# Optimization experiments

Hardware: AMD Instinct MI355X
Metric: run time of the kernel (lower is better)

Reference implementation:

```python
import jax, jax.numpy as jnp
import numpy as np

N = 10000
E = 160000
IN_CH, HID, OUT = 14, 128, 4
HEADS = 8
NEG_SLOPE = 0.2


def setup_inputs() -> dict:
    key = jax.random.key(0)
    ks = jax.random.split(key, 16)
    glorot = lambda k, shape: jax.random.normal(k, shape, jnp.float32) * np.sqrt(2.0 / (shape[0] + shape[-1]))
    inp = {
        'x': jax.random.normal(ks[0], (N, IN_CH), jnp.float32),
        'edge_index': jax.random.randint(ks[1], (2, E), 0, N, jnp.int64),
        # layer 1: 14 -> 8 heads x 128, concat
        'W1': glorot(ks[2], (IN_CH, HEADS * HID)),
        'a_src1': glorot(ks[3], (HEADS, HID)),
        'a_dst1': glorot(ks[4], (HEADS, HID)),
        'b1': jnp.zeros((HEADS * HID,), jnp.float32),
        # layer 2: 1024 -> 8 heads x 128, concat
        'W2': glorot(ks[5], (HEADS * HID, HEADS * HID)),
        'a_src2': glorot(ks[6], (HEADS, HID)),
        'a_dst2': glorot(ks[7], (HEADS, HID)),
        'b2': jnp.zeros((HEADS * HID,), jnp.float32),
        # layer 3: 1024 -> 1 head x 4, mean (concat=False)
        'W3': glorot(ks[8], (HEADS * HID, OUT)),
        'a_src3': glorot(ks[9], (1, OUT)),
        'a_dst3': glorot(ks[10], (1, OUT)),
        'b3': jnp.zeros((OUT,), jnp.float32),
    }
    return inp


def gat_conv(x, src, dst, W, a_src, a_dst, b, heads, out_ch, concat):
    n = x.shape[0]
    h = (x @ W).reshape(n, heads, out_ch)                      # [N,H,C]
    al_s = jnp.sum(h * a_src, axis=-1)                         # [N,H]
    al_d = jnp.sum(h * a_dst, axis=-1)                         # [N,H]
    e = al_s[src] + al_d[dst]                                  # [E,H]
    e = jnp.where(e > 0, e, NEG_SLOPE * e)                     # LeakyReLU(0.2)
    # segment softmax over incoming edges of each dst node
    m = jax.ops.segment_max(e, dst, num_segments=n)
    ex = jnp.exp(e - m[dst])
    z = jax.ops.segment_sum(ex, dst, num_segments=n)
    alpha = ex / (z[dst] + 1e-16)                              # [E,H]
    out = jax.ops.segment_sum(h[src] * alpha[:, :, None], dst, num_segments=n)  # [N,H,C]
    out = out.reshape(n, heads * out_ch) if concat else out.mean(axis=1)
    return out + b


def reference(x, edge_index, W1, a_src1, a_dst1, b1, W2, a_src2, a_dst2, b2, W3, a_src3, a_dst3, b3):
    n = x.shape[0]
    # add self-loops (PyG GATConv default)
    loop = jnp.arange(n, dtype=edge_index.dtype)
    src = jnp.concatenate([edge_index[0], loop])
    dst = jnp.concatenate([edge_index[1], loop])
    # dropout layers are identity in eval mode
    h = gat_conv(x, src, dst, W1, a_src1, a_dst1, b1, HEADS, HID, True)
    h = jax.nn.relu(h)
    h = gat_conv(h, src, dst, W2, a_src2, a_dst2, b2, HEADS, HID, True)
    h = jax.nn.relu(h)
    h = gat_conv(h, src, dst, W3, a_src3, a_dst3, b3, 1, OUT, False)
    h = jax.nn.relu(h)
    return h
```

## Files before the change

kernel.cpp:

```cpp
#include <hip/hip_runtime.h>

typedef unsigned short ushort_t;
typedef unsigned int uint32;

#define N_NODES 10000
#define N_EDGES 160000
#define ET (N_NODES + N_EDGES)
#define MPAD 10112
#define HT 1024
#define HEADS 8
#define NEG 0.2f
#define AGG_CH 64

#define O_FLAG     0
#define O_SRC      256
#define O_DST      (O_SRC + 680192)
#define O_COUNTS   (O_DST + 680192)
#define O_OFFS     (O_COUNTS + 40192)
#define O_CURS     (O_OFFS + 40192)
#define O_SSORT    (O_CURS + 40192)
#define O_ALS      (O_SSORT + 680192)
#define O_ALD      (O_ALS + 320000)
#define O_AL3S     (O_ALD + 320000)
#define O_AL3D     (O_AL3S + 40192)
#define O_H3       (O_AL3D + 40192)
#define O_XF       (O_H3 + 160000)
#define O_W1F      (O_XF + 560128)
#define O_AS1F     (O_W1F + 57344)
#define O_W3F      (O_AS1F + 24576)
#define O_S3F      (O_W3F + 16384)
#define O_W2T      (O_S3F + 768)
#define O_BUFA     (O_W2T + 2097152)
#define O_BUFB     (O_BUFA + 20709376)

__device__ __forceinline__ float bf2f(ushort_t u){ return __uint_as_float(((uint32)u) << 16); }
__device__ __forceinline__ ushort_t f2bf(float f){
    uint32 x = __float_as_uint(f);
    return (ushort_t)((x + 0x7fffu + ((x >> 16) & 1u)) >> 16);
}
__device__ __forceinline__ void unpack2(uint32 u, float& lo, float& hi){
    lo = __uint_as_float(u << 16);
    hi = __uint_as_float(u & 0xffff0000u);
}

typedef __bf16 bf16x8 __attribute__((ext_vector_type(8)));
typedef float  f32x4  __attribute__((ext_vector_type(4)));

typedef const __attribute__((address_space(1))) uint32* gas1_u32;
typedef       __attribute__((address_space(3))) uint32* las3_u32;

__device__ __forceinline__ void gload_lds16(const void* g, void* l){
    __builtin_amdgcn_global_load_lds((gas1_u32)g, (las3_u32)l, 16, 0, 0);
}

__global__ void k_probe(const int* __restrict__ ei, const uint32* __restrict__ w1raw,
                        int* __restrict__ flags){
    if (threadIdx.x == 0){
        int nz = 0;
        for (int i = 0; i < 128; i++) nz |= ei[2*i + 1];
        flags[0] = (nz == 0) ? 1 : 0;
    }
    if (threadIdx.x == 1){
        int cnt = 0;
        for (int i = 0; i < 256; i++){
            uint32 e = (w1raw[i] >> 7) & 0xffu;
            cnt += (e >= 64u && e <= 160u) ? 1 : 0;
        }
        flags[1] = (cnt > 200) ? 0 : 1;
    }
}

struct CvtArgs {
    const void* src[12];
    float*      dst[12];
    int         n[12];
};

__global__ __launch_bounds__(256) void k_cvt(CvtArgs a, const int* __restrict__ flags){
    int aid = blockIdx.y;
    int n = a.n[aid];
    int base = blockIdx.x * 1024 + threadIdx.x * 4;
    if (base >= n) return;
    int f32 = flags[1];
    const void* s = a.src[aid];
    float* d = a.dst[aid];
    #pragma unroll
    for (int j = 0; j < 4; j++){
        int i = base + j;
        if (i < n){
            d[i] = f32 ? ((const float*)s)[i] : bf2f(((const ushort_t*)s)[i]);
        }
    }
}

__global__ __launch_bounds__(256) void k_extract_hist(const void* __restrict__ ei, const int* __restrict__ flags,
                                                      int* __restrict__ src, int* __restrict__ dst,
                                                      int* __restrict__ counts){
    int i = blockIdx.x * 256 + threadIdx.x;
    int is64 = flags[0];
    int s = -1, d = -1;
    if (i < N_EDGES){
        if (is64){
            const long long* p = (const long long*)ei;
            s = (int)p[i]; d = (int)p[N_EDGES + i];
        } else {
            const int* p = (const int*)ei;
            s = p[i]; d = p[N_EDGES + i];
        }
    } else if (i < ET){
        s = i - N_EDGES; d = s;
    }
    if (d >= 0){
        src[i] = s; dst[i] = d;
        atomicAdd(&counts[d], 1);
    }
}

__global__ __launch_bounds__(1024) void k_scan(const int* __restrict__ counts, int* __restrict__ offs,
                                               int* __restrict__ cursors, int n){
    __shared__ int wsum[16];
    __shared__ int running_s;
    int tid = threadIdx.x;
    int lane = tid & 63, wid = tid >> 6;
    if (tid == 0) running_s = 0;
    __syncthreads();
    for (int base = 0; base < n; base += 1024){
        int i = base + tid;
        int v = (i < n) ? counts[i] : 0;
        int x = v;
        #pragma unroll
        for (int d = 1; d < 64; d <<= 1){
            int t = __shfl_up(x, d, 64);
            if (lane >= d) x += t;
        }
        if (lane == 63) wsum[wid] = x;
        __syncthreads();
        if (wid == 0 && lane < 16){
            int w = wsum[lane];
            #pragma unroll
            for (int d = 1; d < 16; d <<= 1){
                int t = __shfl_up(w, d, 64);
                if (lane >= d) w += t;
            }
            wsum[lane] = w;
        }
        __syncthreads();
        int wprefix = (wid == 0) ? 0 : wsum[wid - 1];
        int run = running_s;
        int excl = run + wprefix + (x - v);
        if (i < n){ offs[i] = excl; cursors[i] = excl; }
        __syncthreads();
        if (tid == 0) running_s = run + wsum[15];
        __syncthreads();
    }
    if (tid == 0) offs[n] = running_s;
}

__global__ __launch_bounds__(256) void k_scatter(const int* __restrict__ src, const int* __restrict__ dst,
                                                 int* __restrict__ cursors, int* __restrict__ ssort){
    int i = blockIdx.x * 256 + threadIdx.x;
    if (i < ET){
        int pos = atomicAdd(&cursors[dst[i]], 1);
        ssort[pos] = src[i];
    }
}

__global__ __launch_bounds__(256) void k_gemm1f(const float* __restrict__ x, const float* __restrict__ W1,
                                                const float* __restrict__ a_src, const float* __restrict__ a_dst,
                                                ushort_t* __restrict__ h1,
                                                float* __restrict__ alS, float* __restrict__ alD){
    __shared__ float w1s[14 * HT];
    int tid = threadIdx.x;
    for (int i = tid * 4; i < 14 * HT; i += 1024)
        *(float4*)(w1s + i) = *(const float4*)(W1 + i);
    int c0 = tid * 4;
    float4 sv = *(const float4*)(a_src + c0);
    float4 dv = *(const float4*)(a_dst + c0);
    int head = tid >> 5, l32 = tid & 31;
    __syncthreads();
    for (int n = blockIdx.x; n < N_NODES; n += gridDim.x){
        float a0=0.f, a1=0.f, a2=0.f, a3=0.f;
        #pragma unroll
        for (int k = 0; k < 14; k++){
            float xv = x[n*14 + k];
            float4 w = *(const float4*)(w1s + k*HT + c0);
            a0 += xv*w.x; a1 += xv*w.y; a2 += xv*w.z; a3 += xv*w.w;
        }
        uint2 o;
        o.x = (uint32)f2bf(a0) | ((uint32)f2bf(a1) << 16);
        o.y = (uint32)f2bf(a2) | ((uint32)f2bf(a3) << 16);
        *(uint2*)(h1 + (size_t)n*HT + c0) = o;
        float h0,h1v,h2,h3v;
        unpack2(o.x, h0, h1v); unpack2(o.y, h2, h3v);
        float s = h0*sv.x + h1v*sv.y + h2*sv.z + h3v*sv.w;
        float d = h0*dv.x + h1v*dv.y + h2*dv.z + h3v*dv.w;
        #pragma unroll
        for (int of = 16; of; of >>= 1){ s += __shfl_xor(s, of, 32); d += __shfl_xor(d, of, 32); }
        if (l32 == 0){ alS[n*HEADS + head] = s; alD[n*HEADS + head] = d; }
    }
}

__global__ __launch_bounds__(256) void k_alpha2(const ushort_t* __restrict__ H, const float* __restrict__ a_src,
                                                const float* __restrict__ a_dst,
                                                float* __restrict__ alS, float* __restrict__ alD){
    int tid = threadIdx.x;
    int c0 = tid * 4;
    float4 sv = *(const float4*)(a_src + c0);
    float4 dv = *(const float4*)(a_dst + c0);
    int head = tid >> 5, l32 = tid & 31;
    int n0 = blockIdx.x * 16;
    for (int i = 0; i < 16; i++){
        int n = n0 + i;
        uint2 hv = *(const uint2*)(H + (size_t)n*HT + c0);
        float h0,h1,h2,h3;
        unpack2(hv.x, h0, h1); unpack2(hv.y, h2, h3);
        float s = h0*sv.x + h1*sv.y + h2*sv.z + h3*sv.w;
        float d = h0*dv.x + h1*dv.y + h2*dv.z + h3*dv.w;
        #pragma unroll
        for (int of = 16; of; of >>= 1){ s += __shfl_xor(s, of, 32); d += __shfl_xor(d, of, 32); }
        if (l32 == 0){ alS[n*HEADS + head] = s; alD[n*HEADS + head] = d; }
    }
}

__global__ __launch_bounds__(256) void k_gat_agg(const ushort_t* __restrict__ H, const float* __restrict__ alS,
                                                 const float* __restrict__ alD, const int* __restrict__ offs,
                                                 const int* __restrict__ srcs, const float* __restrict__ bias,
                                                 ushort_t* __restrict__ out){
    int n = blockIdx.x;
    int tid = threadIdx.x;
    int beg = offs[n], end = offs[n+1];
    __shared__ float sm[HEADS], sz[HEADS];
    __shared__ int   sE[AGG_CH];
    __shared__ float wE[AGG_CH][HEADS];
    __shared__ float red[HEADS][128];

    {
        int head32 = tid >> 5, l32 = tid & 31;
        float ad = alD[n*HEADS + head32];
        float m = -1e30f;
        for (int e = beg + l32; e < end; e += 32){
            float v = alS[srcs[e]*HEADS + head32] + ad;
            v = v > 0.f ? v : NEG*v;
            m = fmaxf(m, v);
        }
        #pragma unroll
        for (int o = 16; o; o >>= 1) m = fmaxf(m, __shfl_xor(m, o, 32));
        float z = 0.f;
        for (int e = beg + l32; e < end; e += 32){
            float v = alS[srcs[e]*HEADS + head32] + ad;
            v = v > 0.f ? v : NEG*v;
            z += __expf(v - m);
        }
        #pragma unroll
        for (int o = 16; o; o >>= 1) z += __shfl_xor(z, o, 32);
        if (l32 == 0){ sm[head32] = m; sz[head32] = z; }
    }
    __syncthreads();

    int slot = tid >> 7;
    int lt   = tid & 127;
    int ch0  = lt * 8;
    int head = lt >> 4;
    float acc[8];
    #pragma unroll
    for (int j = 0; j < 8; j++) acc[j] = 0.f;

    for (int cb = beg; cb < end; cb += AGG_CH){
        int cn = min(AGG_CH, end - cb);
        if (tid < cn) sE[tid] = srcs[cb + tid];
        __syncthreads();
        #pragma unroll
        for (int r = 0; r < 2; r++){
            int idx = tid + r*256;
            int e = idx >> 3, hd = idx & 7;
            if (e < cn){
                int s = sE[e];
                float v = alS[s*HEADS + hd] + alD[n*HEADS + hd];
                v = v > 0.f ? v : NEG*v;
                wE[e][hd] = __expf(v - sm[hd]) / (sz[hd] + 1e-16f);
            }
        }
        __syncthreads();
        for (int e = slot; e < cn; e += 2){
            int s = sE[e];
            float w = wE[e][head];
            uint4 hv = *(const uint4*)(H + (size_t)s*HT + ch0);
            float f0,f1,f2,f3,f4,f5,f6,f7;
            unpack2(hv.x, f0, f1); unpack2(hv.y, f2, f3);
            unpack2(hv.z, f4, f5); unpack2(hv.w, f6, f7);
            acc[0]+=w*f0; acc[1]+=w*f1; acc[2]+=w*f2; acc[3]+=w*f3;
            acc[4]+=w*f4; acc[5]+=w*f5; acc[6]+=w*f6; acc[7]+=w*f7;
        }
        __syncthreads();
    }
    if (slot == 1){
        #pragma unroll
        for (int j = 0; j < 8; j++) red[j & 7][lt] = acc[j] + 0.f*red[0][0];
    }
    __syncthreads();
    if (slot == 0){
        #pragma unroll
        for (int j = 0; j < 8; j++) acc[j] += red[j][lt];
        float4 bv0 = *(const float4*)(bias + ch0);
        float4 bv1 = *(const float4*)(bias + ch0 + 4);
        float r0 = fmaxf(acc[0]+bv0.x, 0.f), r1 = fmaxf(acc[1]+bv0.y, 0.f);
        float r2 = fmaxf(acc[2]+bv0.z, 0.f), r3 = fmaxf(acc[3]+bv0.w, 0.f);
        float r4 = fmaxf(acc[4]+bv1.x, 0.f), r5 = fmaxf(acc[5]+bv1.y, 0.f);
        float r6 = fmaxf(acc[6]+bv1.z, 0.f), r7 = fmaxf(acc[7]+bv1.w, 0.f);
        uint4 o;
        o.x = (uint32)f2bf(r0) | ((uint32)f2bf(r1) << 16);
        o.y = (uint32)f2bf(r2) | ((uint32)f2bf(r3) << 16);
        o.z = (uint32)f2bf(r4) | ((uint32)f2bf(r5) << 16);
        o.w = (uint32)f2bf(r6) | ((uint32)f2bf(r7) << 16);
        *(uint4*)(out + (size_t)n*HT + ch0) = o;
    }
}

__global__ __launch_bounds__(256) void k_transpose(const void* __restrict__ in, const int* __restrict__ flags,
                                                   ushort_t* __restrict__ out){
    __shared__ ushort_t tile[32][33];
    int f32 = flags[1];
    int bx = blockIdx.x, by = blockIdx.y;
    int cx = threadIdx.x & 31;
    int ry = (threadIdx.x >> 5) * 4;
    #pragma unroll
    for (int r = 0; r < 4; r++){
        size_t idx = (size_t)(by*32 + ry + r)*1024 + bx*32 + cx;
        tile[ry + r][cx] = f32 ? f2bf(((const float*)in)[idx]) : ((const ushort_t*)in)[idx];
    }
    __syncthreads();
    #pragma unroll
    for (int r = 0; r < 4; r++)
        out[(size_t)(bx*32 + ry + r)*1024 + by*32 + cx] = tile[cx][ry + r];
}

__global__ __launch_bounds__(256) void k_gemm2(const ushort_t* __restrict__ A, const ushort_t* __restrict__ BT,
                                               ushort_t* __restrict__ C){
    __shared__ ushort_t lA[128*32];
    __shared__ ushort_t lB[128*32];
    int tid = threadIdx.x;
    int bm = blockIdx.x, bn = blockIdx.y;
    int lane = tid & 63;
    int wave = tid >> 6;
    int wm = (wave & 1) * 64, wn = (wave >> 1) * 64;
    int lm = lane & 15, kg = lane >> 4;
    f32x4 acc[4][4];
    #pragma unroll
    for (int i = 0; i < 4; i++)
        #pragma unroll
        for (int j = 0; j < 4; j++) acc[i][j] = (f32x4)0.0f;

    const int K = 1024;
    int rowA0 = bm * 128, rowB0 = bn * 128;
    for (int k0 = 0; k0 < K; k0 += 32){
        #pragma unroll
        for (int it = 0; it < 2; ++it){
            int s = tid + it*256;
            int r = s >> 2, ks = s & 3;
            gload_lds16(A  + (size_t)(rowA0 + r)*K + k0 + ks*8, lA + s*8);
            gload_lds16(BT + (size_t)(rowB0 + r)*K + k0 + ks*8, lB + s*8);
        }
        __syncthreads();
        bf16x8 af[4], bfr[4];
        #pragma unroll
        for (int mt = 0; mt < 4; mt++) af[mt]  = *(const bf16x8*)(lA + (wm + mt*16 + lm)*32 + kg*8);
        #pragma unroll
        for (int nt = 0; nt < 4; nt++) bfr[nt] = *(const bf16x8*)(lB + (wn + nt*16 + lm)*32 + kg*8);
        #pragma unroll
        for (int mt = 0; mt < 4; mt++)
            #pragma unroll
            for (int nt = 0; nt < 4; nt++)
                acc[mt][nt] = __builtin_amdgcn_mfma_f32_16x16x32_bf16(af[mt], bfr[nt], acc[mt][nt], 0, 0, 0);
        __syncthreads();
    }
    #pragma unroll
    for (int mt = 0; mt < 4; mt++){
        int row_base = bm*128 + wm + mt*16 + kg*4;
        #pragma unroll
        for (int nt = 0; nt < 4; nt++){
            int col = bn*128 + wn + nt*16 + lm;
            #pragma unroll
            for (int r = 0; r < 4; r++){
                int row = row_base + r;
                if (row < N_NODES) C[(size_t)row*HT + col] = f2bf(acc[mt][nt][r]);
            }
        }
    }
}

__global__ __launch_bounds__(256) void k_gemm3(const ushort_t* __restrict__ A, const float* __restrict__ W3,
                                               const float* __restrict__ s3,
                                               float* __restrict__ h3, float* __restrict__ al3s, float* __restrict__ al3d){
    int tid = threadIdx.x;
    int lane = tid & 63, wave = tid >> 6;
    int n = blockIdx.x * 4 + wave;
    if (n >= N_NODES) return;
    float4 w3r[16];
    #pragma unroll
    for (int j = 0; j < 16; j++) w3r[j] = ((const float4*)W3)[lane*16 + j];
    const uint4* ap = (const uint4*)(A + (size_t)n*HT + lane*16);
    uint4 u0 = ap[0], u1 = ap[1];
    uint32 uu[8] = {u0.x,u0.y,u0.z,u0.w,u1.x,u1.y,u1.z,u1.w};
    float acc0=0.f, acc1=0.f, acc2=0.f, acc3=0.f;
    #pragma unroll
    for (int p = 0; p < 8; p++){
        float lo, hi;
        unpack2(uu[p], lo, hi);
        float4 wl = w3r[p*2], wh = w3r[p*2+1];
        acc0 += lo*wl.x + hi*wh.x;
        acc1 += lo*wl.y + hi*wh.y;
        acc2 += lo*wl.z + hi*wh.z;
        acc3 += lo*wl.w + hi*wh.w;
    }
    #pragma unroll
    for (int o = 32; o; o >>= 1){
        acc0 += __shfl_xor(acc0, o, 64); acc1 += __shfl_xor(acc1, o, 64);
        acc2 += __shfl_xor(acc2, o, 64); acc3 += __shfl_xor(acc3, o, 64);
    }
    if (lane == 0){
        *(float4*)(h3 + n*4) = make_float4(acc0, acc1, acc2, acc3);
        al3s[n] = acc0*s3[0] + acc1*s3[1] + acc2*s3[2] + acc3*s3[3];
        al3d[n] = acc0*s3[16] + acc1*s3[17] + acc2*s3[18] + acc3*s3[19];
    }
}

__global__ __launch_bounds__(256) void k_gat_agg3(const float* __restrict__ h3, const float* __restrict__ al3s,
                                                  const float* __restrict__ al3d, const int* __restrict__ offs,
                                                  const int* __restrict__ srcs, const float* __restrict__ b3,
                                                  const int* __restrict__ flags, void* __restrict__ out){
    int tid = threadIdx.x;
    int l = tid & 63, wave = tid >> 6;
    int n = blockIdx.x * 4 + wave;
    if (n >= N_NODES) return;
    int beg = offs[n], end = offs[n+1];
    float ad = al3d[n];
    float m = -1e30f;
    for (int e = beg + l; e < end; e += 64){
        float v = al3s[srcs[e]] + ad; v = v > 0.f ? v : NEG*v;
        m = fmaxf(m, v);
    }
    #pragma unroll
    for (int o = 32; o; o >>= 1) m = fmaxf(m, __shfl_xor(m, o, 64));
    float z = 0.f;
    for (int e = beg + l; e < end; e += 64){
        float v = al3s[srcs[e]] + ad; v = v > 0.f ? v : NEG*v;
        z += __expf(v - m);
    }
    #pragma unroll
    for (int o = 32; o; o >>= 1) z += __shfl_xor(z, o, 64);
    float inv = 1.f / (z + 1e-16f);
    float a0=0.f, a1=0.f, a2=0.f, a3=0.f;
    for (int e = beg + l; e < end; e += 64){
        int s = srcs[e];
        float v = al3s[s] + ad; v = v > 0.f ? v : NEG*v;
        float w = __expf(v - m) * inv;
        float4 hv = *(const float4*)(h3 + s*4);
        a0 += w*hv.x; a1 += w*hv.y; a2 += w*hv.z; a3 += w*hv.w;
    }
    #pragma unroll
    for (int o = 32; o; o >>= 1){
        a0 += __shfl_xor(a0, o, 64); a1 += __shfl_xor(a1, o, 64);
        a2 += __shfl_xor(a2, o, 64); a3 += __shfl_xor(a3, o, 64);
    }
    if (l == 0){
        float r0 = fmaxf(a0 + b3[0], 0.f);
        float r1 = fmaxf(a1 + b3[1], 0.f);
        float r2 = fmaxf(a2 + b3[2], 0.f);
        float r3 = fmaxf(a3 + b3[3], 0.f);
        if (flags[1]){
            float* o4 = (float*)out;
            o4[n*4+0]=r0; o4[n*4+1]=r1; o4[n*4+2]=r2; o4[n*4+3]=r3;
        } else {
            ushort_t* o2 = (ushort_t*)out;
            o2[n*4+0]=f2bf(r0); o2[n*4+1]=f2bf(r1); o2[n*4+2]=f2bf(r2); o2[n*4+3]=f2bf(r3);
        }
    }
}

extern "C" void kernel_launch(void* const* d_in, const int* in_sizes, int n_in,
                              void* d_out, int out_size, void* d_ws, size_t ws_size,
                              hipStream_t stream){
    const void* x   = d_in[0];
    const void* ei  = d_in[1];
    const void* W1  = d_in[2];
    const void* as1 = d_in[3];
    const void* ad1 = d_in[4];
    const void* b1  = d_in[5];
    const void* W2  = d_in[6];
    const void* as2 = d_in[7];
    const void* ad2 = d_in[8];
    const void* b2  = d_in[9];
    const void* W3  = d_in[10];
    const void* as3 = d_in[11];
    const void* ad3 = d_in[12];
    const void* b3  = d_in[13];

    char* ws = (char*)d_ws;
    int* flags     = (int*)(ws + O_FLAG);
    int* srcA      = (int*)(ws + O_SRC);
    int* dstA      = (int*)(ws + O_DST);
    int* counts    = (int*)(ws + O_COUNTS);
    int* offs      = (int*)(ws + O_OFFS);
    int* cursors   = (int*)(ws + O_CURS);
    int* ssort     = (int*)(ws + O_SSORT);
    float* alS     = (float*)(ws + O_ALS);
    float* alD     = (float*)(ws + O_ALD);
    float* al3s    = (float*)(ws + O_AL3S);
    float* al3d    = (float*)(ws + O_AL3D);
    float* h3      = (float*)(ws + O_H3);
    float* xF      = (float*)(ws + O_XF);
    float* W1F     = (float*)(ws + O_W1F);
    float* wvecF   = (float*)(ws + O_AS1F);
    float* W3F     = (float*)(ws + O_W3F);
    float* s3F     = (float*)(ws + O_S3F);
    ushort_t* W2T  = (ushort_t*)(ws + O_W2T);
    ushort_t* bufA = (ushort_t*)(ws + O_BUFA);
    ushort_t* bufB = (ushort_t*)(ws + O_BUFB);

    const int EB = (ET + 255) / 256;

    k_probe<<<1, 64, 0, stream>>>((const int*)ei, (const uint32*)W1, flags);

    CvtArgs ca;
    ca.src[0]=x;   ca.dst[0]=xF;            ca.n[0]=140000;
    ca.src[1]=W1;  ca.dst[1]=W1F;           ca.n[1]=14336;
    ca.src[2]=as1; ca.dst[2]=wvecF+0*1024;  ca.n[2]=1024;
    ca.src[3]=ad1; ca.dst[3]=wvecF+1*1024;  ca.n[3]=1024;
    ca.src[4]=b1;  ca.dst[4]=wvecF+2*1024;  ca.n[4]=1024;
    ca.src[5]=as2; ca.dst[5]=wvecF+3*1024;  ca.n[5]=1024;
    ca.src[6]=ad2; ca.dst[6]=wvecF+4*1024;  ca.n[6]=1024;
    ca.src[7]=b2;  ca.dst[7]=wvecF+5*1024;  ca.n[7]=1024;
    ca.src[8]=W3;  ca.dst[8]=W3F;           ca.n[8]=4096;
    ca.src[9]=as3; ca.dst[9]=s3F+0;         ca.n[9]=4;
    ca.src[10]=ad3; ca.dst[10]=s3F+16;      ca.n[10]=4;
    ca.src[11]=b3;  ca.dst[11]=s3F+32;      ca.n[11]=4;
    k_cvt<<<dim3(137, 12), 256, 0, stream>>>(ca, flags);

    hipMemsetAsync(counts, 0, N_NODES*sizeof(int), stream);
    k_extract_hist<<<EB, 256, 0, stream>>>(ei, flags, srcA, dstA, counts);
    k_scan<<<1, 1024, 0, stream>>>(counts, offs, cursors, N_NODES);
    k_scatter<<<EB, 256, 0, stream>>>(srcA, dstA, cursors, ssort);

    k_gemm1f<<<512, 256, 0, stream>>>(xF, W1F, wvecF+0*1024, wvecF+1*1024, bufA, alS, alD);
    k_gat_agg<<<N_NODES, 256, 0, stream>>>(bufA, alS, alD, offs, ssort, wvecF+2*1024, bufB);

    k_transpose<<<dim3(32, 32), 256, 0, stream>>>(W2, flags, W2T);
    k_gemm2<<<dim3(79, 8), 256, 0, stream>>>(bufB, W2T, bufA);
    k_alpha2<<<625, 256, 0, stream>>>(bufA, wvecF+3*1024, wvecF+4*1024, alS, alD);
    k_gat_agg<<<N_NODES, 256, 0, stream>>>(bufA, alS, alD, offs, ssort, wvecF+5*1024, bufB);

    k_gemm3<<<2500, 256, 0, stream>>>(bufB, W3F, s3F, h3, al3s, al3d);
    k_gat_agg3<<<2500, 256, 0, stream>>>(h3, al3s, al3d, offs, ssort, s3F+32, flags, d_out);
}
```

Measured before the change: 334.5 us.

## Fuse setup kernels, fold alpha into GEMM2, rewrite GAT aggregation with online softmax

Merges the probe, conversion, counts memset and W2 transpose into one setup kernel, so fewer launches are serialized. The per-node attention logits for layer 2 are now computed in the GEMM2 epilogue from fp32 accumulators, which removes the separate alpha pass over H. The aggregation kernel is rewritten to use two waves per node with shuffle-broadcast sources and an online max/sum softmax, avoiding LDS staging and block barriers. Risks include redundant probe_f32 work in every setup block and an extra reduction and barrier in the GEMM2 epilogue.

```diff
diff --git a/kernel.cpp b/kernel.cpp
--- a/kernel.cpp
+++ b/kernel.cpp
@@ -10,7 +10,6 @@
 #define HT 1024
 #define HEADS 8
 #define NEG 0.2f
-#define AGG_CH 64
 
 #define O_FLAG     0
 #define O_SRC      256
@@ -53,21 +52,18 @@
     __builtin_amdgcn_global_load_lds((gas1_u32)g, (las3_u32)l, 16, 0, 0);
 }
 
-__global__ void k_probe(const int* __restrict__ ei, const uint32* __restrict__ w1raw,
-                        int* __restrict__ flags){
-    if (threadIdx.x == 0){
-        int nz = 0;
-        for (int i = 0; i < 128; i++) nz |= ei[2*i + 1];
-        flags[0] = (nz == 0) ? 1 : 0;
-    }
-    if (threadIdx.x == 1){
-        int cnt = 0;
-        for (int i = 0; i < 256; i++){
-            uint32 e = (w1raw[i] >> 7) & 0xffu;
-            cnt += (e >= 64u && e <= 160u) ? 1 : 0;
-        }
-        flags[1] = (cnt > 200) ? 0 : 1;
-    }
+__device__ __forceinline__ int probe_f32(const uint32* __restrict__ w){
+    int cnt = 0;
+    for (int i = 0; i < 256; i++){
+        uint32 e = (w[i] >> 7) & 0xffu;
+        cnt += (e >= 64u && e <= 160u) ? 1 : 0;
+    }
+    return (cnt > 200) ? 0 : 1;
+}
+__device__ __forceinline__ int probe_edge64(const int* __restrict__ ei){
+    int nz = 0;
+    for (int i = 0; i < 128; i++) nz |= ei[2*i + 1];
+    return (nz == 0) ? 1 : 0;
 }
 
 struct CvtArgs {
@@ -76,20 +72,55 @@
     int         n[12];
 };
 
-__global__ __launch_bounds__(256) void k_cvt(CvtArgs a, const int* __restrict__ flags){
-    int aid = blockIdx.y;
-    int n = a.n[aid];
-    int base = blockIdx.x * 1024 + threadIdx.x * 4;
-    if (base >= n) return;
-    int f32 = flags[1];
-    const void* s = a.src[aid];
-    float* d = a.dst[aid];
-    #pragma unroll
-    for (int j = 0; j < 4; j++){
-        int i = base + j;
-        if (i < n){
-            d[i] = f32 ? ((const float*)s)[i] : bf2f(((const ushort_t*)s)[i]);
-        }
+__global__ __launch_bounds__(256) void k_setup(CvtArgs a, const void* __restrict__ W2,
+                                               const uint32* __restrict__ w1raw,
+                                               const int* __restrict__ eiraw,
+                                               int* __restrict__ counts,
+                                               ushort_t* __restrict__ W2T,
+                                               int* __restrict__ flags){
+    __shared__ ushort_t tile[32][33];
+    int slice = blockIdx.y;
+    int tid = threadIdx.x;
+    if (slice < 12){
+        int n = a.n[slice];
+        int base = blockIdx.x * 1024 + tid * 4;
+        if (base >= n) return;
+        int f32 = probe_f32(w1raw);
+        const void* s = a.src[slice];
+        float* d = a.dst[slice];
+        #pragma unroll
+        for (int j = 0; j < 4; j++){
+            int i = base + j;
+            if (i < n) d[i] = f32 ? ((const float*)s)[i] : bf2f(((const ushort_t*)s)[i]);
+        }
+    } else if (slice == 12){
+        if (blockIdx.x == 10){
+            if (tid == 0) flags[0] = probe_edge64(eiraw);
+            if (tid == 1) flags[1] = probe_f32(w1raw);
+            return;
+        }
+        if (blockIdx.x < 10){
+            int i0 = blockIdx.x * 1024 + tid * 4;
+            if (i0 + 3 < N_NODES){
+                *(int4*)(counts + i0) = make_int4(0,0,0,0);
+            } else {
+                for (int j = 0; j < 4; j++) if (i0 + j < N_NODES) counts[i0 + j] = 0;
+            }
+        }
+    } else {
+        int f32 = probe_f32(w1raw);
+        int bx = blockIdx.x & 31, by = blockIdx.x >> 5;
+        int cx = tid & 31;
+        int ry = (tid >> 5) * 4;
+        #pragma unroll
+        for (int r = 0; r < 4; r++){
+            size_t idx = (size_t)(by*32 + ry + r)*1024 + bx*32 + cx;
+            tile[ry + r][cx] = f32 ? f2bf(((const float*)W2)[idx]) : ((const ushort_t*)W2)[idx];
+        }
+        __syncthreads();
+        #pragma unroll
+        for (int r = 0; r < 4; r++)
+            W2T[(size_t)(bx*32 + ry + r)*1024 + by*32 + cx] = tile[cx][ry + r];
     }
 }
 
@@ -200,144 +231,100 @@
     }
 }
 
-__global__ __launch_bounds__(256) void k_alpha2(const ushort_t* __restrict__ H, const float* __restrict__ a_src,
-                                                const float* __restrict__ a_dst,
-                                                float* __restrict__ alS, float* __restrict__ alD){
-    int tid = threadIdx.x;
-    int c0 = tid * 4;
-    float4 sv = *(const float4*)(a_src + c0);
-    float4 dv = *(const float4*)(a_dst + c0);
-    int head = tid >> 5, l32 = tid & 31;
-    int n0 = blockIdx.x * 16;
-    for (int i = 0; i < 16; i++){
-        int n = n0 + i;
-        uint2 hv = *(const uint2*)(H + (size_t)n*HT + c0);
-        float h0,h1,h2,h3;
-        unpack2(hv.x, h0, h1); unpack2(hv.y, h2, h3);
-        float s = h0*sv.x + h1*sv.y + h2*sv.z + h3*sv.w;
-        float d = h0*dv.x + h1*dv.y + h2*dv.z + h3*dv.w;
-        #pragma unroll
-        for (int of = 16; of; of >>= 1){ s += __shfl_xor(s, of, 32); d += __shfl_xor(d, of, 32); }
-        if (l32 == 0){ alS[n*HEADS + head] = s; alD[n*HEADS + head] = d; }
-    }
-}
-
 __global__ __launch_bounds__(256) void k_gat_agg(const ushort_t* __restrict__ H, const float* __restrict__ alS,
                                                  const float* __restrict__ alD, const int* __restrict__ offs,
                                                  const int* __restrict__ srcs, const float* __restrict__ bias,
                                                  ushort_t* __restrict__ out){
-    int n = blockIdx.x;
-    int tid = threadIdx.x;
+    int tid = threadIdx.x;
+    int wv = tid >> 6, lane = tid & 63;
+    int n = blockIdx.x * 2 + (wv >> 1);
+    int half = wv & 1;
     int beg = offs[n], end = offs[n+1];
-    __shared__ float sm[HEADS], sz[HEADS];
-    __shared__ int   sE[AGG_CH];
-    __shared__ float wE[AGG_CH][HEADS];
-    __shared__ float red[HEADS][128];
-
-    {
-        int head32 = tid >> 5, l32 = tid & 31;
-        float ad = alD[n*HEADS + head32];
-        float m = -1e30f;
-        for (int e = beg + l32; e < end; e += 32){
-            float v = alS[srcs[e]*HEADS + head32] + ad;
+    int head = half*4 + (lane >> 4);
+    int slot = lane & 15;
+    float ad = alD[n*HEADS + head];
+
+    float m = -1e30f, z = 0.f;
+    for (int c = beg; c < end; c += 64){
+        int cn = min(64, end - c);
+        int sreg = (lane < cn) ? srcs[c + lane] : 0;
+        for (int p = slot; p < cn; p += 16){
+            int s = __shfl(sreg, p, 64);
+            float v = alS[s*HEADS + head] + ad;
             v = v > 0.f ? v : NEG*v;
-            m = fmaxf(m, v);
-        }
-        #pragma unroll
-        for (int o = 16; o; o >>= 1) m = fmaxf(m, __shfl_xor(m, o, 32));
-        float z = 0.f;
-        for (int e = beg + l32; e < end; e += 32){
-            float v = alS[srcs[e]*HEADS + head32] + ad;
-            v = v > 0.f ? v : NEG*v;
-            z += __expf(v - m);
-        }
-        #pragma unroll
-        for (int o = 16; o; o >>= 1) z += __shfl_xor(z, o, 32);
-        if (l32 == 0){ sm[head32] = m; sz[head32] = z; }
-    }
-    __syncthreads();
-
-    int slot = tid >> 7;
-    int lt   = tid & 127;
-    int ch0  = lt * 8;
-    int head = lt >> 4;
-    float acc[8];
-    #pragma unroll
-    for (int j = 0; j < 8; j++) acc[j] = 0.f;
-
-    for (int cb = beg; cb < end; cb += AGG_CH){
-        int cn = min(AGG_CH, end - cb);
-        if (tid < cn) sE[tid] = srcs[cb + tid];
-        __syncthreads();
-        #pragma unroll
-        for (int r = 0; r < 2; r++){
-            int idx = tid + r*256;
-            int e = idx >> 3, hd = idx & 7;
-            if (e < cn){
-                int s = sE[e];
-                float v = alS[s*HEADS + hd] + alD[n*HEADS + hd];
-                v = v > 0.f ? v : NEG*v;
-                wE[e][hd] = __expf(v - sm[hd]) / (sz[hd] + 1e-16f);
-            }
-        }
-        __syncthreads();
-        for (int e = slot; e < cn; e += 2){
-            int s = sE[e];
-            float w = wE[e][head];
-            uint4 hv = *(const uint4*)(H + (size_t)s*HT + ch0);
+            if (v > m){ z = z*__expf(m - v) + 1.f; m = v; }
+            else z += __expf(v - m);
+        }
+    }
+    #pragma unroll
+    for (int o = 1; o < 16; o <<= 1){
+        float m2 = __shfl_xor(m, o, 64);
+        float z2 = __shfl_xor(z, o, 64);
+        float nm = fmaxf(m, m2);
+        z = z*__expf(m - nm) + z2*__expf(m2 - nm);
+        m = nm;
+    }
+    float inv = 1.f / (z + 1e-16f);
+
+    int ch0 = half*512 + lane*8;
+    const ushort_t* Hc = H + ch0;
+    float c0=0.f,c1=0.f,c2=0.f,c3=0.f,c4=0.f,c5=0.f,c6=0.f,c7=0.f;
+    for (int c = beg; c < end; c += 64){
+        int cn = min(64, end - c);
+        int sreg = (lane < cn) ? srcs[c + lane] : 0;
+        int j = 0;
+        for (; j + 2 <= cn; j += 2){
+            int s0 = __shfl(sreg, j, 64);
+            int s1 = __shfl(sreg, j+1, 64);
+            uint4 u0 = *(const uint4*)(Hc + (size_t)s0*HT);
+            uint4 u1 = *(const uint4*)(Hc + (size_t)s1*HT);
+            float v0 = alS[s0*HEADS + head] + ad;
+            float v1 = alS[s1*HEADS + head] + ad;
+            v0 = v0 > 0.f ? v0 : NEG*v0;
+            v1 = v1 > 0.f ? v1 : NEG*v1;
+            float w0 = __expf(v0 - m) * inv;
+            float w1 = __expf(v1 - m) * inv;
             float f0,f1,f2,f3,f4,f5,f6,f7;
-            unpack2(hv.x, f0, f1); unpack2(hv.y, f2, f3);
-            unpack2(hv.z, f4, f5); unpack2(hv.w, f6, f7);
-            acc[0]+=w*f0; acc[1]+=w*f1; acc[2]+=w*f2; acc[3]+=w*f3;
-            acc[4]+=w*f4; acc[5]+=w*f5; acc[6]+=w*f6; acc[7]+=w*f7;
-        }
-        __syncthreads();
-    }
-    if (slot == 1){
-        #pragma unroll
-        for (int j = 0; j < 8; j++) red[j & 7][lt] = acc[j] + 0.f*red[0][0];
-    }
-    __syncthreads();
-    if (slot == 0){
-        #pragma unroll
-        for (int j = 0; j < 8; j++) acc[j] += red[j][lt];
-        float4 bv0 = *(const float4*)(bias + ch0);
-        float4 bv1 = *(const float4*)(bias + ch0 + 4);
-        float r0 = fmaxf(acc[0]+bv0.x, 0.f), r1 = fmaxf(acc[1]+bv0.y, 0.f);
-        float r2 = fmaxf(acc[2]+bv0.z, 0.f), r3 = fmaxf(acc[3]+bv0.w, 0.f);
-        float r4 = fmaxf(acc[4]+bv1.x, 0.f), r5 = fmaxf(acc[5]+bv1.y, 0.f);
-        float r6 = fmaxf(acc[6]+bv1.z, 0.f), r7 = fmaxf(acc[7]+bv1.w, 0.f);
-        uint4 o;
-        o.x = (uint32)f2bf(r0) | ((uint32)f2bf(r1) << 16);
-        o.y = (uint32)f2bf(r2) | ((uint32)f2bf(r3) << 16);
-        o.z = (uint32)f2bf(r4) | ((uint32)f2bf(r5) << 16);
-        o.w = (uint32)f2bf(r6) | ((uint32)f2bf(r7) << 16);
-        *(uint4*)(out + (size_t)n*HT + ch0) = o;
-    }
-}
-
-__global__ __launch_bounds__(256) void k_transpose(const void* __restrict__ in, const int* __restrict__ flags,
-                                                   ushort_t* __restrict__ out){
-    __shared__ ushort_t tile[32][33];
-    int f32 = flags[1];
-    int bx = blockIdx.x, by = blockIdx.y;
-    int cx = threadIdx.x & 31;
-    int ry = (threadIdx.x >> 5) * 4;
-    #pragma unroll
-    for (int r = 0; r < 4; r++){
-        size_t idx = (size_t)(by*32 + ry + r)*1024 + bx*32 + cx;
-        tile[ry + r][cx] = f32 ? f2bf(((const float*)in)[idx]) : ((const ushort_t*)in)[idx];
-    }
-    __syncthreads();
-    #pragma unroll
-    for (int r = 0; r < 4; r++)
-        out[(size_t)(bx*32 + ry + r)*1024 + by*32 + cx] = tile[cx][ry + r];
+            unpack2(u0.x,f0,f1); unpack2(u0.y,f2,f3); unpack2(u0.z,f4,f5); unpack2(u0.w,f6,f7);
+            c0+=w0*f0; c1+=w0*f1; c2+=w0*f2; c3+=w0*f3;
+            c4+=w0*f4; c5+=w0*f5; c6+=w0*f6; c7+=w0*f7;
+            unpack2(u1.x,f0,f1); unpack2(u1.y,f2,f3); unpack2(u1.z,f4,f5); unpack2(u1.w,f6,f7);
+            c0+=w1*f0; c1+=w1*f1; c2+=w1*f2; c3+=w1*f3;
+            c4+=w1*f4; c5+=w1*f5; c6+=w1*f6; c7+=w1*f7;
+        }
+        if (j < cn){
+            int s0 = __shfl(sreg, j, 64);
+            uint4 u0 = *(const uint4*)(Hc + (size_t)s0*HT);
+            float v0 = alS[s0*HEADS + head] + ad;
+            v0 = v0 > 0.f ? v0 : NEG*v0;
+            float w0 = __expf(v0 - m) * inv;
+            float f0,f1,f2,f3,f4,f5,f6,f7;
+            unpack2(u0.x,f0,f1); unpack2(u0.y,f2,f3); unpack2(u0.z,f4,f5); unpack2(u0.w,f6,f7);
+            c0+=w0*f0; c1+=w0*f1; c2+=w0*f2; c3+=w0*f3;
+            c4+=w0*f4; c5+=w0*f5; c6+=w0*f6; c7+=w0*f7;
+        }
+    }
+    float4 b0 = *(const float4*)(bias + ch0);
+    float4 b1 = *(const float4*)(bias + ch0 + 4);
+    c0 = fmaxf(c0+b0.x, 0.f); c1 = fmaxf(c1+b0.y, 0.f);
+    c2 = fmaxf(c2+b0.z, 0.f); c3 = fmaxf(c3+b0.w, 0.f);
+    c4 = fmaxf(c4+b1.x, 0.f); c5 = fmaxf(c5+b1.y, 0.f);
+    c6 = fmaxf(c6+b1.z, 0.f); c7 = fmaxf(c7+b1.w, 0.f);
+    uint4 o;
+    o.x = (uint32)f2bf(c0) | ((uint32)f2bf(c1) << 16);
+    o.y = (uint32)f2bf(c2) | ((uint32)f2bf(c3) << 16);
+    o.z = (uint32)f2bf(c4) | ((uint32)f2bf(c5) << 16);
+    o.w = (uint32)f2bf(c6) | ((uint32)f2bf(c7) << 16);
+    *(uint4*)(out + (size_t)n*HT + ch0) = o;
 }
 
 __global__ __launch_bounds__(256) void k_gemm2(const ushort_t* __restrict__ A, const ushort_t* __restrict__ BT,
-                                               ushort_t* __restrict__ C){
+                                               ushort_t* __restrict__ C,
+                                               const float* __restrict__ aS, const float* __restrict__ aD,
+                                               float* __restrict__ alS, float* __restrict__ alD){
     __shared__ ushort_t lA[128*32];
     __shared__ ushort_t lB[128*32];
+    __shared__ float reds[2][64][2];
     int tid = threadIdx.x;
     int bm = blockIdx.x, bn = blockIdx.y;
     int lane = tid & 63;
@@ -383,6 +370,46 @@
             for (int r = 0; r < 4; r++){
                 int row = row_base + r;
                 if (row < N_NODES) C[(size_t)row*HT + col] = f2bf(acc[mt][nt][r]);
+            }
+        }
+    }
+    float as_l[4], ad_l[4];
+    #pragma unroll
+    for (int nt = 0; nt < 4; nt++){
+        as_l[nt] = aS[bn*128 + wn + nt*16 + lm];
+        ad_l[nt] = aD[bn*128 + wn + nt*16 + lm];
+    }
+    float psA[4][4], pdA[4][4];
+    #pragma unroll
+    for (int mt = 0; mt < 4; mt++){
+        #pragma unroll
+        for (int r = 0; r < 4; r++){
+            float ps = acc[mt][0][r]*as_l[0] + acc[mt][1][r]*as_l[1]
+                     + acc[mt][2][r]*as_l[2] + acc[mt][3][r]*as_l[3];
+            float pd = acc[mt][0][r]*ad_l[0] + acc[mt][1][r]*ad_l[1]
+                     + acc[mt][2][r]*ad_l[2] + acc[mt][3][r]*ad_l[3];
+            #pragma unroll
+            for (int o = 1; o < 16; o <<= 1){ ps += __shfl_xor(ps, o, 64); pd += __shfl_xor(pd, o, 64); }
+            psA[mt][r] = ps; pdA[mt][r] = pd;
+            if (wn == 64 && lm == 0){
+                int rl = mt*16 + kg*4 + r;
+                reds[wm >> 6][rl][0] = ps;
+                reds[wm >> 6][rl][1] = pd;
+            }
+        }
+    }
+    __syncthreads();
+    if (wn == 0 && lm == 0){
+        #pragma unroll
+        for (int mt = 0; mt < 4; mt++){
+            #pragma unroll
+            for (int r = 0; r < 4; r++){
+                int rl = mt*16 + kg*4 + r;
+                int row = bm*128 + wm + rl;
+                if (row < N_NODES){
+                    alS[row*HEADS + bn] = psA[mt][r] + reds[wm >> 6][rl][0];
+                    alD[row*HEADS + bn] = pdA[mt][r] + reds[wm >> 6][rl][1];
+                }
             }
         }
     }
@@ -519,8 +546,6 @@
 
     const int EB = (ET + 255) / 256;
 
-    k_probe<<<1, 64, 0, stream>>>((const int*)ei, (const uint32*)W1, flags);
-
     CvtArgs ca;
     ca.src[0]=x;   ca.dst[0]=xF;            ca.n[0]=140000;
     ca.src[1]=W1;  ca.dst[1]=W1F;           ca.n[1]=14336;
@@ -534,20 +559,18 @@
     ca.src[9]=as3; ca.dst[9]=s3F+0;         ca.n[9]=4;
     ca.src[10]=ad3; ca.dst[10]=s3F+16;      ca.n[10]=4;
     ca.src[11]=b3;  ca.dst[11]=s3F+32;      ca.n[11]=4;
-    k_cvt<<<dim3(137, 12), 256, 0, stream>>>(ca, flags);
-
-    hipMemsetAsync(counts, 0, N_NODES*sizeof(int), stream);
+
+    k_setup<<<dim3(1024, 14), 256, 0, stream>>>(ca, W2, (const uint32*)W1, (const int*)ei,
+                                                counts, W2T, flags);
     k_extract_hist<<<EB, 256, 0, stream>>>(ei, flags, srcA, dstA, counts);
     k_scan<<<1, 1024, 0, stream>>>(counts, offs, cursors, N_NODES);
     k_scatter<<<EB, 256, 0, stream>>>(srcA, dstA, cursors, ssort);
 
     k_gemm1f<<<512, 256, 0, stream>>>(xF, W1F, wvecF+0*1024, wvecF+1*1024, bufA, alS, alD);
-    k_gat_agg<<<N_NODES, 256, 0, stream>>>(bufA, alS, alD, offs, ssort, wvecF+2*1024, bufB);
-
-    k_transpose<<<dim3(32, 32), 256, 0, stream>>>(W2, flags, W2T);
-    k_gemm2<<<dim3(79, 8), 256, 0, stream>>>(bufB, W2T, bufA);
-    k_alpha2<<<625, 256, 0, stream>>>(bufA, wvecF+3*1024, wvecF+4*1024, alS, alD);
-    k_gat_agg<<<N_NODES, 256, 0, stream>>>(bufA, alS, alD, offs, ssort, wvecF+5*1024, bufB);
+    k_gat_agg<<<5000, 256, 0, stream>>>(bufA, alS, alD, offs, ssort, wvecF+2*1024, bufB);
+
+    k_gemm2<<<dim3(79, 8), 256, 0, stream>>>(bufB, W2T, bufA, wvecF+3*1024, wvecF+4*1024, alS, alD);
+    k_gat_agg<<<5000, 256, 0, stream>>>(bufA, alS, alD, offs, ssort, wvecF+5*1024, bufB);
 
     k_gemm3<<<2500, 256, 0, stream>>>(bufB, W3F, s3F, h3, al3s, al3d);
     k_gat_agg3<<<2500, 256, 0, stream>>>(h3, al3s, al3d, offs, ssort, s3F+32, flags, d_out);
```

New measurement: 339.9 us. No clear change (+1.6%).
